# Optimization experiments

Measured on AMD Instinct MI355X. Metric: run time of the kernel, lower is better.

Reference implementation:

```python
import jax, jax.numpy as jnp
import numpy as np
from jax import lax

SCOPE = 15
RICKER_WIDTH = 3.0
DAMP = 0.12
MAX_STEPS = 10


def mexican_hat(scope, width, damping):
    # ricker / mexican-hat wavelet sampled at `scope` integer-spaced points, scaled by damping
    x = np.linspace(-(scope // 2), scope // 2, scope).astype(np.float32)
    norm = 2.0 / (np.sqrt(3.0 * width) * np.pi ** 0.25)
    w = damping * norm * (1.0 - (x / width) ** 2) * np.exp(-(x ** 2) / (2.0 * width ** 2))
    return jnp.asarray(w, dtype=jnp.float32)


def setup_inputs() -> dict:
    key = jax.random.key(0)
    activations = jax.random.normal(key, (32, 256, 56, 56), dtype=jnp.float32)
    w_rec = mexican_hat(SCOPE, RICKER_WIDTH, DAMP)  # [scope]
    return {"activations": activations, "w_rec": w_rec, "max_steps": MAX_STEPS}


def reference(activations, w_rec, max_steps):
    # activations: [B, C, H, W]; inhibition conv runs along the C axis only.
    scope = w_rec.shape[0]
    pad = scope // 2
    x = activations[:, None]                     # [B, 1, C, H, W]
    kernel = w_rec.reshape(1, 1, scope, 1, 1)    # OIDHW

    def conv(y):
        return lax.conv_general_dilated(
            y, kernel,
            window_strides=(1, 1, 1),
            padding=[(pad, pad), (0, 0), (0, 0)],
            dimension_numbers=("NCDHW", "OIDHW", "NCDHW"),
        )

    # fixed-point iteration: state <- activations + W_rec * state  (threshold=0 => always max_steps iters)
    state = x
    for _ in range(max_steps):
        state = x + conv(state)
    return state[:, 0]  # squeeze channel dim -> [B, C, H, W]
```

## Files before the change

kernel.cpp:

```cpp
#include <hip/hip_runtime.h>


#define NCH 256
#define PAD 7
#define SCOPE 15
#define SPATIAL 3136
#define PER_B 802816
#define STW 32
#define STILES_PER_B 98
#define GRID_APPLY 224
#define NITER 14
#define MAXCH 12

typedef __attribute__((ext_vector_type(8))) __bf16 bf16x8;
typedef __attribute__((ext_vector_type(16))) float float16;
typedef __attribute__((ext_vector_type(4))) unsigned int uint4v;

static __device__ __forceinline__ unsigned short f2bf_rn_u(float f) {
  unsigned u = __builtin_bit_cast(unsigned int, f);
  return (unsigned short)((u + 0x7FFFu + ((u >> 16) & 1u)) >> 16);
}
static __device__ __forceinline__ float bf2f_u(unsigned short h) {
  unsigned u = ((unsigned)h) << 16;
  return __builtin_bit_cast(float, u);
}
static __device__ __forceinline__ unsigned pack_bf2(float a, float b) {
  return (unsigned)f2bf_rn_u(a) | ((unsigned)f2bf_rn_u(b) << 16);
}

__global__ void build_M_kernel(const float* __restrict__ w,
                               const int* __restrict__ max_steps_p,
                               unsigned short* __restrict__ Mh,
                               unsigned short* __restrict__ Ml) {
  const int d = blockIdx.x;
  const int c = threadIdx.x;
  __shared__ float v[2][NCH];
  __shared__ float wsh[SCOPE];
  if (c < SCOPE) wsh[c] = w[c];
  const float e = (c == d) ? 1.0f : 0.0f;
  v[0][c] = e;
  __syncthreads();
  const int steps = *max_steps_p;
  int cur = 0;
  for (int t = 0; t < steps; ++t) {
    float s = e;
#pragma unroll
    for (int j = 0; j < SCOPE; ++j) {
      const int cc = c + j - PAD;
      if (cc >= 0 && cc < NCH) s += wsh[j] * v[cur][cc];
    }
    cur ^= 1;
    v[cur][c] = s;
    __syncthreads();
  }
  const float f = v[cur][c];
  const unsigned short h = f2bf_rn_u(f);
  Mh[c * NCH + d] = h;
  Ml[c * NCH + d] = f2bf_rn_u(f - bf2f_u(h));
}

__global__ __launch_bounds__(512, 2) void apply_M_kernel(
    const float* __restrict__ x, const unsigned short* __restrict__ Mh,
    const unsigned short* __restrict__ Ml, float* __restrict__ out) {
  __shared__ float tile[2][NCH * STW];

  const int tid  = threadIdx.x;
  const int lane = tid & 63;
  const int w    = tid >> 6;
  const int m    = lane & 31;
  const int half = lane >> 5;
  const int c0   = w * 32;

  int tlo = c0 - 70;
  if (tlo < 0) tlo = 0;
  tlo >>= 4;
  if (tlo > 4) tlo = 4;

  bf16x8 Ah[MAXCH], Al[MAXCH];
  {
    const int abase = (c0 + m) * NCH + half * 8;
#pragma unroll
    for (int i = 0; i < MAXCH; ++i) {
      const int off = abase + (tlo + i) * 16;
      Ah[i] = *(const bf16x8*)(Mh + off);
      Al[i] = *(const bf16x8*)(Ml + off);
    }
  }

  const int srow = lane >> 3;
  const int scol = (lane & 7) * 4;

  int tau = (int)blockIdx.x;
  int b   = tau / STILES_PER_B;
  int s0  = (tau % STILES_PER_B) * STW;

  {
    const float* gb = x + (size_t)b * PER_B + (size_t)s0;
#pragma unroll
    for (int r = 0; r < 4; ++r) {
      const int d0 = w * 32 + r * 8;
      const float* g = gb + (size_t)(d0 + srow) * SPATIAL + scol;
      __builtin_amdgcn_global_load_lds(
          (const __attribute__((address_space(1))) unsigned int*)g,
          (__attribute__((address_space(3))) unsigned int*)&tile[0][d0 * STW],
          16, 0, 0);
    }
  }

#pragma unroll 1
  for (int it = 0; it < NITER; ++it) {
    const int cur  = it & 1;
    const int more = (it + 1 < NITER) ? 1 : 0;
    const int ntau = tau + GRID_APPLY;
    const int nb   = more ? (ntau / STILES_PER_B) : 0;
    const int ns0  = more ? (ntau % STILES_PER_B) * STW : 0;

    __syncthreads();

    if (more) {
      const float* gb = x + (size_t)nb * PER_B + (size_t)ns0;
#pragma unroll
      for (int r = 0; r < 4; ++r) {
        const int d0 = w * 32 + r * 8;
        const float* g = gb + (size_t)(d0 + srow) * SPATIAL + scol;
        __builtin_amdgcn_global_load_lds(
            (const __attribute__((address_space(1))) unsigned int*)g,
            (__attribute__((address_space(3))) unsigned int*)&tile[1 - cur][d0 * STW],
            16, 0, 0);
      }
    }

    const float* tb = &tile[cur][0];
    float16 acc;
#pragma unroll
    for (int q = 0; q < 16; ++q) acc[q] = 0.0f;

#pragma unroll
    for (int i = 0; i < MAXCH; ++i) {
      const int dk = (tlo + i) * 16 + half * 8;
      const float* p = tb + dk * STW + m;
      const float v0 = p[0 * STW], v1 = p[1 * STW], v2 = p[2 * STW],
                  v3 = p[3 * STW], v4 = p[4 * STW], v5 = p[5 * STW],
                  v6 = p[6 * STW], v7 = p[7 * STW];

      const unsigned uh0 = pack_bf2(v0, v1);
      const unsigned uh1 = pack_bf2(v2, v3);
      const unsigned uh2 = pack_bf2(v4, v5);
      const unsigned uh3 = pack_bf2(v6, v7);

      const float r0 = v0 - __builtin_bit_cast(float, uh0 << 16);
      const float r1 = v1 - __builtin_bit_cast(float, uh0 & 0xFFFF0000u);
      const float r2 = v2 - __builtin_bit_cast(float, uh1 << 16);
      const float r3 = v3 - __builtin_bit_cast(float, uh1 & 0xFFFF0000u);
      const float r4 = v4 - __builtin_bit_cast(float, uh2 << 16);
      const float r5 = v5 - __builtin_bit_cast(float, uh2 & 0xFFFF0000u);
      const float r6 = v6 - __builtin_bit_cast(float, uh3 << 16);
      const float r7 = v7 - __builtin_bit_cast(float, uh3 & 0xFFFF0000u);

      const unsigned ul0 = pack_bf2(r0, r1);
      const unsigned ul1 = pack_bf2(r2, r3);
      const unsigned ul2 = pack_bf2(r4, r5);
      const unsigned ul3 = pack_bf2(r6, r7);

      const uint4v vh = {uh0, uh1, uh2, uh3};
      const uint4v vl = {ul0, ul1, ul2, ul3};
      const bf16x8 bh = __builtin_bit_cast(bf16x8, vh);
      const bf16x8 bl = __builtin_bit_cast(bf16x8, vl);

      acc = __builtin_amdgcn_mfma_f32_32x32x16_bf16(Ah[i], bh, acc, 0, 0, 0);
      acc = __builtin_amdgcn_mfma_f32_32x32x16_bf16(Ah[i], bl, acc, 0, 0, 0);
      acc = __builtin_amdgcn_mfma_f32_32x32x16_bf16(Al[i], bh, acc, 0, 0, 0);
    }

    float* ob = out + (size_t)b * PER_B + (size_t)s0 + m;
#pragma unroll
    for (int r = 0; r < 16; ++r) {
      const int row = (r & 3) + 8 * (r >> 2) + 4 * half;
      ob[(size_t)(c0 + row) * SPATIAL] = acc[r];
    }

    tau = ntau;
    b = nb;
    s0 = ns0;
  }
}

extern "C" void kernel_launch(void* const* d_in, const int* in_sizes, int n_in,
                              void* d_out, int out_size, void* d_ws, size_t ws_size,
                              hipStream_t stream) {
  const float* x = (const float*)d_in[0];
  const float* w = (const float*)d_in[1];
  const int* ms = (const int*)d_in[2];
  float* out = (float*)d_out;

  unsigned short* Mh = (unsigned short*)d_ws;
  unsigned short* Ml = Mh + NCH * NCH;

  build_M_kernel<<<NCH, NCH, 0, stream>>>(w, ms, Mh, Ml);
  apply_M_kernel<<<GRID_APPLY, 512, 0, stream>>>(x, Mh, Ml, out);
}
```

Baseline: 206.9 us.

## Split activations to bf16 hi/lo once per tile in LDS, skip zero band chunks

The bf16 hi/lo split of each activation tile is now done once per block, and the packed halves are stored in LDS. Before, every wave redid the split for its own chunks. Prefetch moves from async global_load_lds to register float4 loads. The grid becomes 256 blocks striding over 3136 tiles. The MFMA K-chunks are limited to the nonzero band of M, so edge waves do less work, and three independent accumulators break the MFMA dependency chain. The trade-offs are extra registers for the prefetch, two barriers per tile, and uneven tile counts across blocks (3136/256 is not whole).

```diff
diff --git a/kernel.cpp b/kernel.cpp
--- a/kernel.cpp
+++ b/kernel.cpp
@@ -8,8 +8,8 @@
 #define PER_B 802816
 #define STW 32
 #define STILES_PER_B 98
-#define GRID_APPLY 224
-#define NITER 14
+#define NTILES 3136
+#define GRID_APPLY 256
 #define MAXCH 12
 
 typedef __attribute__((ext_vector_type(8))) __bf16 bf16x8;
@@ -26,6 +26,13 @@
 }
 static __device__ __forceinline__ unsigned pack_bf2(float a, float b) {
   return (unsigned)f2bf_rn_u(a) | ((unsigned)f2bf_rn_u(b) << 16);
+}
+static __device__ __forceinline__ void split2(float a, float b,
+                                              unsigned& h, unsigned& l) {
+  h = pack_bf2(a, b);
+  const float ra = a - __builtin_bit_cast(float, h << 16);
+  const float rb = b - __builtin_bit_cast(float, h & 0xFFFF0000u);
+  l = pack_bf2(ra, rb);
 }
 
 __global__ void build_M_kernel(const float* __restrict__ w,
@@ -62,7 +69,8 @@
 __global__ __launch_bounds__(512, 2) void apply_M_kernel(
     const float* __restrict__ x, const unsigned short* __restrict__ Mh,
     const unsigned short* __restrict__ Ml, float* __restrict__ out) {
-  __shared__ float tile[2][NCH * STW];
+  __shared__ unsigned HB[128 * STW];
+  __shared__ unsigned LB[128 * STW];
 
   const int tid  = threadIdx.x;
   const int lane = tid & 63;
@@ -71,117 +79,90 @@
   const int half = lane >> 5;
   const int c0   = w * 32;
 
-  int tlo = c0 - 70;
-  if (tlo < 0) tlo = 0;
-  tlo >>= 4;
-  if (tlo > 4) tlo = 4;
+  int clo = c0 - 70; if (clo < 0) clo = 0; clo >>= 4;
+  int chi = c0 + 101; if (chi > 255) chi = 255; chi >>= 4;
+  const int nch = chi - clo + 1;
 
   bf16x8 Ah[MAXCH], Al[MAXCH];
-  {
-    const int abase = (c0 + m) * NCH + half * 8;
 #pragma unroll
-    for (int i = 0; i < MAXCH; ++i) {
-      const int off = abase + (tlo + i) * 16;
+  for (int i = 0; i < MAXCH; ++i) {
+    if (i < nch) {
+      const int off = (c0 + m) * NCH + (clo + i) * 16 + half * 8;
       Ah[i] = *(const bf16x8*)(Mh + off);
       Al[i] = *(const bf16x8*)(Ml + off);
     }
   }
 
-  const int srow = lane >> 3;
-  const int scol = (lane & 7) * 4;
+  const int sq = (tid & 7) * 4;
+  const int dg = tid >> 3;
 
-  int tau = (int)blockIdx.x;
-  int b   = tau / STILES_PER_B;
-  int s0  = (tau % STILES_PER_B) * STW;
-
+  int tau = blockIdx.x;
+  float4 g0, g1, g2, g3;
   {
-    const float* gb = x + (size_t)b * PER_B + (size_t)s0;
-#pragma unroll
-    for (int r = 0; r < 4; ++r) {
-      const int d0 = w * 32 + r * 8;
-      const float* g = gb + (size_t)(d0 + srow) * SPATIAL + scol;
-      __builtin_amdgcn_global_load_lds(
-          (const __attribute__((address_space(1))) unsigned int*)g,
-          (__attribute__((address_space(3))) unsigned int*)&tile[0][d0 * STW],
-          16, 0, 0);
-    }
+    const float* gb = x + (size_t)(tau / STILES_PER_B) * PER_B
+                        + (size_t)(tau % STILES_PER_B) * STW;
+    g0 = *(const float4*)(gb + (size_t)(2 * dg) * SPATIAL + sq);
+    g1 = *(const float4*)(gb + (size_t)(2 * dg + 1) * SPATIAL + sq);
+    g2 = *(const float4*)(gb + (size_t)(2 * dg + 128) * SPATIAL + sq);
+    g3 = *(const float4*)(gb + (size_t)(2 * dg + 129) * SPATIAL + sq);
   }
 
 #pragma unroll 1
-  for (int it = 0; it < NITER; ++it) {
-    const int cur  = it & 1;
-    const int more = (it + 1 < NITER) ? 1 : 0;
+  for (; tau < NTILES; tau += GRID_APPLY) {
+    __syncthreads();
+
+    {
+      unsigned h0, h1, h2, h3, l0, l1, l2, l3;
+      split2(g0.x, g1.x, h0, l0); split2(g0.y, g1.y, h1, l1);
+      split2(g0.z, g1.z, h2, l2); split2(g0.w, g1.w, h3, l3);
+      *(uint4v*)&HB[dg * STW + sq] = (uint4v){h0, h1, h2, h3};
+      *(uint4v*)&LB[dg * STW + sq] = (uint4v){l0, l1, l2, l3};
+      split2(g2.x, g3.x, h0, l0); split2(g2.y, g3.y, h1, l1);
+      split2(g2.z, g3.z, h2, l2); split2(g2.w, g3.w, h3, l3);
+      *(uint4v*)&HB[(dg + 64) * STW + sq] = (uint4v){h0, h1, h2, h3};
+      *(uint4v*)&LB[(dg + 64) * STW + sq] = (uint4v){l0, l1, l2, l3};
+    }
+
     const int ntau = tau + GRID_APPLY;
-    const int nb   = more ? (ntau / STILES_PER_B) : 0;
-    const int ns0  = more ? (ntau % STILES_PER_B) * STW : 0;
+    if (ntau < NTILES) {
+      const float* gb = x + (size_t)(ntau / STILES_PER_B) * PER_B
+                          + (size_t)(ntau % STILES_PER_B) * STW;
+      g0 = *(const float4*)(gb + (size_t)(2 * dg) * SPATIAL + sq);
+      g1 = *(const float4*)(gb + (size_t)(2 * dg + 1) * SPATIAL + sq);
+      g2 = *(const float4*)(gb + (size_t)(2 * dg + 128) * SPATIAL + sq);
+      g3 = *(const float4*)(gb + (size_t)(2 * dg + 129) * SPATIAL + sq);
+    }
 
     __syncthreads();
 
-    if (more) {
-      const float* gb = x + (size_t)nb * PER_B + (size_t)ns0;
+    float16 a0, a1, a2;
 #pragma unroll
-      for (int r = 0; r < 4; ++r) {
-        const int d0 = w * 32 + r * 8;
-        const float* g = gb + (size_t)(d0 + srow) * SPATIAL + scol;
-        __builtin_amdgcn_global_load_lds(
-            (const __attribute__((address_space(1))) unsigned int*)g,
-            (__attribute__((address_space(3))) unsigned int*)&tile[1 - cur][d0 * STW],
-            16, 0, 0);
+    for (int q = 0; q < 16; ++q) { a0[q] = 0.0f; a1[q] = 0.0f; a2[q] = 0.0f; }
+
+#pragma unroll
+    for (int i = 0; i < MAXCH; ++i) {
+      if (i < nch) {
+        const int k2b = (clo + i) * 8 + half * 4;
+        const unsigned* hp = &HB[k2b * STW + m];
+        const unsigned* lp = &LB[k2b * STW + m];
+        const uint4v hw = {hp[0], hp[32], hp[64], hp[96]};
+        const uint4v lw = {lp[0], lp[32], lp[64], lp[96]};
+        const bf16x8 bh = __builtin_bit_cast(bf16x8, hw);
+        const bf16x8 bl = __builtin_bit_cast(bf16x8, lw);
+        a0 = __builtin_amdgcn_mfma_f32_32x32x16_bf16(Ah[i], bh, a0, 0, 0, 0);
+        a1 = __builtin_amdgcn_mfma_f32_32x32x16_bf16(Ah[i], bl, a1, 0, 0, 0);
+        a2 = __builtin_amdgcn_mfma_f32_32x32x16_bf16(Al[i], bh, a2, 0, 0, 0);
       }
     }
 
-    const float* tb = &tile[cur][0];
-    float16 acc;
-#pragma unroll
-    for (int q = 0; q < 16; ++q) acc[q] = 0.0f;
-
-#pragma unroll
-    for (int i = 0; i < MAXCH; ++i) {
-      const int dk = (tlo + i) * 16 + half * 8;
-      const float* p = tb + dk * STW + m;
-      const float v0 = p[0 * STW], v1 = p[1 * STW], v2 = p[2 * STW],
-                  v3 = p[3 * STW], v4 = p[4 * STW], v5 = p[5 * STW],
-                  v6 = p[6 * STW], v7 = p[7 * STW];
-
-      const unsigned uh0 = pack_bf2(v0, v1);
-      const unsigned uh1 = pack_bf2(v2, v3);
-      const unsigned uh2 = pack_bf2(v4, v5);
-      const unsigned uh3 = pack_bf2(v6, v7);
-
-      const float r0 = v0 - __builtin_bit_cast(float, uh0 << 16);
-      const float r1 = v1 - __builtin_bit_cast(float, uh0 & 0xFFFF0000u);
-      const float r2 = v2 - __builtin_bit_cast(float, uh1 << 16);
-      const float r3 = v3 - __builtin_bit_cast(float, uh1 & 0xFFFF0000u);
-      const float r4 = v4 - __builtin_bit_cast(float, uh2 << 16);
-      const float r5 = v5 - __builtin_bit_cast(float, uh2 & 0xFFFF0000u);
-      const float r6 = v6 - __builtin_bit_cast(float, uh3 << 16);
-      const float r7 = v7 - __builtin_bit_cast(float, uh3 & 0xFFFF0000u);
-
-      const unsigned ul0 = pack_bf2(r0, r1);
-      const unsigned ul1 = pack_bf2(r2, r3);
-      const unsigned ul2 = pack_bf2(r4, r5);
-      const unsigned ul3 = pack_bf2(r6, r7);
-
-      const uint4v vh = {uh0, uh1, uh2, uh3};
-      const uint4v vl = {ul0, ul1, ul2, ul3};
-      const bf16x8 bh = __builtin_bit_cast(bf16x8, vh);
-      const bf16x8 bl = __builtin_bit_cast(bf16x8, vl);
-
-      acc = __builtin_amdgcn_mfma_f32_32x32x16_bf16(Ah[i], bh, acc, 0, 0, 0);
-      acc = __builtin_amdgcn_mfma_f32_32x32x16_bf16(Ah[i], bl, acc, 0, 0, 0);
-      acc = __builtin_amdgcn_mfma_f32_32x32x16_bf16(Al[i], bh, acc, 0, 0, 0);
-    }
-
+    const int b  = tau / STILES_PER_B;
+    const int s0 = (tau % STILES_PER_B) * STW;
     float* ob = out + (size_t)b * PER_B + (size_t)s0 + m;
 #pragma unroll
     for (int r = 0; r < 16; ++r) {
       const int row = (r & 3) + 8 * (r >> 2) + 4 * half;
-      ob[(size_t)(c0 + row) * SPATIAL] = acc[r];
+      ob[(size_t)(c0 + row) * SPATIAL] = a0[r] + a1[r] + a2[r];
     }
-
-    tau = ntau;
-    b = nb;
-    s0 = ns0;
   }
 }
 
```

New measurement: 205.1 us. About the same (-0.9%).
